# Optimization experiments

Hardware: AMD Instinct MI355X
Metric: run time of the kernel (lower is better)

The kernel has to match this reference:

```python
import jax, jax.numpy as jnp
import numpy as np

N = 50000          # total nodes
N_USER = 40000     # main (user) nodes
E = 400000         # edges per node kind
K = 3              # node kinds (separate graphs)
H = 4              # attention heads
F_IN = 128         # n_units[0]
F_OUT = 64         # n_units[1]
NB_CLASSES = 40
SLOPE = 0.2        # leaky relu negative slope


def setup_inputs() -> dict:
    key = jax.random.key(0)
    ks = jax.random.split(key, 12)
    h = jax.random.normal(ks[0], (N, F_IN), dtype=jnp.float32)
    edge_index = jax.random.randint(ks[1], (K, 2, E), 0, N, dtype=jnp.int32)
    # per-kind SpGATLayer params (bias=False)
    w = jax.random.normal(ks[2], (K, H, F_IN, F_OUT), dtype=jnp.float32) * 0.1
    a_src = jax.random.normal(ks[3], (K, H, F_OUT), dtype=jnp.float32) * 0.1
    a_trg = jax.random.normal(ks[4], (K, H, F_OUT), dtype=jnp.float32) * 0.1
    # AdditiveAttention: w1 (d=F_IN -> d2=F_OUT), w2 (d1=F_OUT -> d2=F_OUT), m (d2 -> 1)
    w1 = jax.random.normal(ks[5], (F_IN, F_OUT), dtype=jnp.float32) * 0.1
    w2 = jax.random.normal(ks[6], (F_OUT, F_OUT), dtype=jnp.float32) * 0.1
    m = jax.random.normal(ks[7], (F_OUT,), dtype=jnp.float32) * 0.1
    # final fc: in = F_OUT*(K+1)
    fc_w = jax.random.normal(ks[8], (F_OUT * (K + 1), NB_CLASSES), dtype=jnp.float32) * 0.1
    fc_b = jnp.zeros((NB_CLASSES,), dtype=jnp.float32)
    return {"h": h, "edge_index": edge_index, "w": w, "a_src": a_src,
            "a_trg": a_trg, "w1": w1, "w2": w2, "m": m,
            "fc_w": fc_w, "fc_b": fc_b}


def _spgat_kind(h, src, trg, wk, ask, atk):
    # h: [N, F_IN], wk: [H, F_IN, F_OUT], ask/atk: [H, F_OUT]
    hp = jnp.einsum('nd,hdf->nhf', h, wk)               # [N, H, F_OUT]
    s = jnp.einsum('nhf,hf->nh', hp, ask)               # [N, H]
    t = jnp.einsum('nhf,hf->nh', hp, atk)               # [N, H]
    e = s[src] + t[trg]                                 # [E, H]
    e = jnp.where(e >= 0, e, SLOPE * e)                 # leaky relu
    e = e - jnp.max(e)                                  # global max shift (as in source)
    exp_e = jnp.exp(e)
    denom = jax.ops.segment_sum(exp_e, trg, num_segments=N)  # [N, H]
    alpha = exp_e / (denom[trg] + 1e-16)                # [E, H]
    msg = hp[src] * alpha[:, :, None]                   # [E, H, F_OUT]
    out = jax.ops.segment_sum(msg, trg, num_segments=N) # [N, H, F_OUT]
    return out.mean(axis=1)                             # [N, F_OUT] (last layer head-mean)


def reference(h, edge_index, w, a_src, a_trg, w1, w2, m, fc_w, fc_b):
    heter = []
    for k in range(K):  # fixed small loop over node kinds
        x = _spgat_kind(h, edge_index[k, 0], edge_index[k, 1],
                        w[k], a_src[k], a_trg[k])
        heter.append(x[:N_USER])
    type_aware = jnp.stack(heter, axis=1)               # [N_USER, K, F_OUT]
    feature = h[:N_USER]                                # [N_USER, F_IN]
    q = jnp.tanh((feature @ w1)[:, None, :] + type_aware @ w2)  # [N_USER, K, F_OUT]
    scores = q @ m                                      # [N_USER, K]
    beta = jax.nn.softmax(scores, axis=-1)
    fusion = jnp.einsum('nk,nkf->nf', beta, type_aware) # [N_USER, F_OUT]
    ret = jnp.concatenate([type_aware, fusion[:, None, :]], axis=1)
    ret = ret.reshape(N_USER, -1)                       # [N_USER, F_OUT*(K+1)]
    logits = ret @ fc_w + fc_b
    return jax.nn.log_softmax(logits, axis=-1)
```

## Files before the change

kernel.cpp:

```cpp
#include <hip/hip_runtime.h>
#include <hip/hip_bf16.h>

#define NN    50000
#define NUSER 40000
#define EE    400000
#define KKIND 3
#define HHEAD 4
#define FIN   128
#define FOUT  64
#define NCLS  40

typedef __attribute__((ext_vector_type(8))) short short8;
typedef __attribute__((ext_vector_type(4))) float floatx4;

__device__ __forceinline__ float bf2f(unsigned short u) {
    unsigned int v = ((unsigned int)u) << 16;
    return __uint_as_float(v);
}
__device__ __forceinline__ unsigned short f2bf(float f) {
    unsigned int u = __float_as_uint(f);
    unsigned int r = (u + 0x7FFFu + ((u >> 16) & 1u)) >> 16;
    return (unsigned short)r;
}

#define OFF_H    0
#define OFF_W    6400000
#define OFF_ASRC 6498304
#define OFF_ATRG 6499072
#define OFF_W1   6499840
#define OFF_W2   6508032
#define OFF_M    6512128
#define OFF_FCW  6512192
#define OFF_FCB  6522432
#define CONV_TOT 6522472

__global__ __launch_bounds__(256) void detect_kernel(const unsigned short* __restrict__ hraw,
                                                     int* __restrict__ flag)
{
    __shared__ int cnt;
    if (threadIdx.x == 0) cnt = 0;
    __syncthreads();
    int local = 0;
#pragma unroll
    for (int j = 0; j < 8; j++) {
        unsigned short u = hraw[threadIdx.x * 8 + j];
        int ex = (u >> 7) & 0xFF;
        if (ex >= 0x90) local++;
    }
    atomicAdd(&cnt, local);
    __syncthreads();
    if (threadIdx.x == 0) *flag = (cnt > 100) ? 1 : 0;
}

__global__ __launch_bounds__(256) void conv_kernel(const void* __restrict__ p0, const void* __restrict__ p2,
                                                   const void* __restrict__ p3, const void* __restrict__ p4,
                                                   const void* __restrict__ p5, const void* __restrict__ p6,
                                                   const void* __restrict__ p7, const void* __restrict__ p8,
                                                   const void* __restrict__ p9,
                                                   const int* __restrict__ flagp,
                                                   unsigned short* __restrict__ dst)
{
    int tid = (blockIdx.x * 256 + threadIdx.x) * 8;
    if (tid >= CONV_TOT) return;
    const void* src; int li;
    if      (tid < OFF_W)    { src = p0; li = tid - OFF_H; }
    else if (tid < OFF_ASRC) { src = p2; li = tid - OFF_W; }
    else if (tid < OFF_ATRG) { src = p3; li = tid - OFF_ASRC; }
    else if (tid < OFF_W1)   { src = p4; li = tid - OFF_ATRG; }
    else if (tid < OFF_W2)   { src = p5; li = tid - OFF_W1; }
    else if (tid < OFF_M)    { src = p6; li = tid - OFF_W2; }
    else if (tid < OFF_FCW)  { src = p7; li = tid - OFF_M; }
    else if (tid < OFF_FCB)  { src = p8; li = tid - OFF_FCW; }
    else                     { src = p9; li = tid - OFF_FCB; }
    if (*flagp) {
        const float* fp = (const float*)src + li;
        float4 x = *(const float4*)fp;
        float4 y = *(const float4*)(fp + 4);
        uint4 o;
        o.x = (unsigned int)f2bf(x.x) | ((unsigned int)f2bf(x.y) << 16);
        o.y = (unsigned int)f2bf(x.z) | ((unsigned int)f2bf(x.w) << 16);
        o.z = (unsigned int)f2bf(y.x) | ((unsigned int)f2bf(y.y) << 16);
        o.w = (unsigned int)f2bf(y.z) | ((unsigned int)f2bf(y.w) << 16);
        *(uint4*)(dst + tid) = o;
    } else {
        *(uint4*)(dst + tid) = *(const uint4*)((const unsigned short*)src + li);
    }
}

__global__ __launch_bounds__(256) void repack_w(const unsigned short* __restrict__ w,
                                                unsigned short* __restrict__ wT)
{
    int tid = blockIdx.x * 256 + threadIdx.x;
    if (tid >= 12288) return;
    int f = tid & 63, g = (tid >> 6) & 15, h = (tid >> 10) & 3, k = tid >> 12;
    const unsigned short* src = w + (size_t)(k * 4 + h) * 8192 + f;
    unsigned short* dst = wT + (size_t)tid * 8;
#pragma unroll
    for (int j = 0; j < 8; j++) dst[j] = src[(size_t)(g * 8 + j) * 64];
}

__global__ __launch_bounds__(256) void repack_small(const unsigned short* __restrict__ w1,
                                                    const unsigned short* __restrict__ w2,
                                                    const unsigned short* __restrict__ fcw,
                                                    unsigned short* __restrict__ w1T,
                                                    unsigned short* __restrict__ w2T,
                                                    unsigned short* __restrict__ fcwT)
{
    int tid = blockIdx.x * 256 + threadIdx.x;
    if (tid < 1024) {
        int c = tid & 63, g = tid >> 6;
#pragma unroll
        for (int j = 0; j < 8; j++) w1T[(size_t)(g * 64 + c) * 8 + j] = w1[(size_t)(g * 8 + j) * 64 + c];
    } else if (tid < 1536) {
        int t = tid - 1024; int c = t & 63, g = t >> 6;
#pragma unroll
        for (int j = 0; j < 8; j++) w2T[(size_t)(g * 64 + c) * 8 + j] = w2[(size_t)(g * 8 + j) * 64 + c];
    } else if (tid < 3072) {
        int t = tid - 1536; int c = t % 48, g = t / 48;
#pragma unroll
        for (int j = 0; j < 8; j++)
            fcwT[(size_t)(g * 48 + c) * 8 + j] = (c < NCLS) ? fcw[(size_t)(g * 8 + j) * NCLS + c] : (unsigned short)0;
    }
}

__global__ __launch_bounds__(256) void hist3(const int* __restrict__ ei,
                                             unsigned int* __restrict__ cnt,
                                             unsigned int* __restrict__ rank)
{
    int e = blockIdx.x * 256 + threadIdx.x;
    int k = blockIdx.y;
    if (e >= EE) return;
    int tn = ei[(size_t)k * 2 * EE + EE + e];
    if (tn < NUSER)
        rank[(size_t)k * EE + e] = atomicAdd(&cnt[(size_t)k * NUSER + tn], 1u);
}

#define SCB 20
__global__ __launch_bounds__(256) void scanA(const unsigned int* __restrict__ cnt,
                                             unsigned int* __restrict__ partials)
{
    int k = blockIdx.y, b = blockIdx.x;
    const unsigned int* c = cnt + (size_t)k * NUSER;
    int base = b * 2048 + threadIdx.x * 8;
    unsigned int s = 0;
#pragma unroll
    for (int j = 0; j < 8; j++) { int idx = base + j; if (idx < NUSER) s += c[idx]; }
#pragma unroll
    for (int off = 1; off < 64; off <<= 1) s += __shfl_xor(s, off, 64);
    __shared__ unsigned int wsum[4];
    int lane = threadIdx.x & 63, wid = threadIdx.x >> 6;
    if (lane == 0) wsum[wid] = s;
    __syncthreads();
    if (threadIdx.x == 0) partials[k * SCB + b] = wsum[0] + wsum[1] + wsum[2] + wsum[3];
}

__global__ __launch_bounds__(256) void scanB(unsigned int* __restrict__ partials,
                                             unsigned int* __restrict__ rowptr)
{
    int wid = threadIdx.x >> 6, lane = threadIdx.x & 63;
    if (wid >= KKIND) return;
    unsigned int v = (lane < SCB) ? partials[wid * SCB + lane] : 0u;
    unsigned int inc = v;
#pragma unroll
    for (int off = 1; off < 32; off <<= 1) {
        unsigned int u = __shfl_up(inc, off, 64);
        if (lane >= off) inc += u;
    }
    if (lane < SCB) partials[wid * SCB + lane] = inc - v;
    if (lane == SCB - 1) rowptr[(size_t)wid * (NUSER + 1) + NUSER] = inc;
}

__global__ __launch_bounds__(256) void scanC(const unsigned int* __restrict__ cnt,
                                             const unsigned int* __restrict__ partials,
                                             unsigned int* __restrict__ rowptr)
{
    int k = blockIdx.y, b = blockIdx.x;
    const unsigned int* c = cnt + (size_t)k * NUSER;
    unsigned int* rp = rowptr + (size_t)k * (NUSER + 1);
    int lane = threadIdx.x & 63, wid = threadIdx.x >> 6;
    int base = b * 2048 + threadIdx.x * 8;
    unsigned int vals[8]; unsigned int s = 0;
#pragma unroll
    for (int j = 0; j < 8; j++) { int idx = base + j; vals[j] = (idx < NUSER) ? c[idx] : 0u; s += vals[j]; }
    unsigned int inc = s;
#pragma unroll
    for (int off = 1; off < 64; off <<= 1) {
        unsigned int u = __shfl_up(inc, off, 64);
        if (lane >= off) inc += u;
    }
    __shared__ unsigned int wsum[4];
    if (lane == 63) wsum[wid] = inc;
    __syncthreads();
    unsigned int woff = 0;
    for (int i = 0; i < wid; i++) woff += wsum[i];
    unsigned int run = partials[k * SCB + b] + woff + (inc - s);
#pragma unroll
    for (int j = 0; j < 8; j++) {
        int idx = base + j;
        if (idx < NUSER) { rp[idx] = run; run += vals[j]; }
    }
}

__global__ __launch_bounds__(256) void scatter3(const int* __restrict__ ei,
                                                const unsigned int* __restrict__ rowptr,
                                                const unsigned int* __restrict__ rank,
                                                int* __restrict__ srcl)
{
    int e = blockIdx.x * 256 + threadIdx.x;
    int k = blockIdx.y;
    if (e >= EE) return;
    const int* srcA = ei + (size_t)k * 2 * EE;
    int tn = srcA[EE + e];
    if (tn >= NUSER) return;
    unsigned int p = rowptr[(size_t)k * (NUSER + 1) + tn] + rank[(size_t)k * EE + e];
    srcl[(size_t)k * EE + p] = srcA[e];
}

__global__ __launch_bounds__(256) void hp_gemm(const unsigned short* __restrict__ h,
                                               const unsigned short* __restrict__ wTk,
                                               const unsigned short* __restrict__ ak_src,
                                               const unsigned short* __restrict__ ak_trg,
                                               unsigned short* __restrict__ hp2,
                                               float* __restrict__ sb, float* __restrict__ tb)
{
    int wave = (blockIdx.x * 256 + threadIdx.x) >> 6;
    int lane = threadIdx.x & 63;
    if (wave >= NN / 16) return;
    int m0 = wave * 16;
    int mi = lane & 15, quad = lane >> 4;

    short8 a[4];
    const unsigned short* hrow = h + (size_t)(m0 + mi) * FIN + quad * 8;
#pragma unroll
    for (int kk = 0; kk < 4; kk++) a[kk] = *(const short8*)(hrow + kk * 32);

    float sp[4][4], tp[4][4];
#pragma unroll
    for (int r = 0; r < 4; r++)
#pragma unroll
        for (int q2 = 0; q2 < 4; q2++) { sp[r][q2] = 0.f; tp[r][q2] = 0.f; }

#pragma unroll
    for (int j = 0; j < 4; j++) {
        int fc = j * 16 + mi;
        floatx4 acc4[4];
#pragma unroll
        for (int hh = 0; hh < 4; hh++) {
            floatx4 acc = {0.f, 0.f, 0.f, 0.f};
#pragma unroll
            for (int kk = 0; kk < 4; kk++) {
                short8 b = *(const short8*)(wTk + (size_t)((hh * 16 + kk * 4 + quad) * 64 + fc) * 8);
                acc = __builtin_amdgcn_mfma_f32_16x16x32_bf16(a[kk], b, acc, 0, 0, 0);
            }
            acc4[hh] = acc;
            float asv = bf2f(ak_src[hh * 64 + fc]);
            float atv = bf2f(ak_trg[hh * 64 + fc]);
#pragma unroll
            for (int reg = 0; reg < 4; reg++) {
                sp[reg][hh] += acc[reg] * asv;
                tp[reg][hh] += acc[reg] * atv;
            }
        }
#pragma unroll
        for (int reg = 0; reg < 4; reg++) {
            ushort4 pk;
            pk.x = f2bf(acc4[0][reg]); pk.y = f2bf(acc4[1][reg]);
            pk.z = f2bf(acc4[2][reg]); pk.w = f2bf(acc4[3][reg]);
            int row = m0 + quad * 4 + reg;
            *(ushort4*)(hp2 + (size_t)row * 256 + fc * 4) = pk;
        }
    }
#pragma unroll
    for (int off = 1; off < 16; off <<= 1)
#pragma unroll
        for (int r = 0; r < 4; r++)
#pragma unroll
            for (int q2 = 0; q2 < 4; q2++) {
                sp[r][q2] += __shfl_xor(sp[r][q2], off, 64);
                tp[r][q2] += __shfl_xor(tp[r][q2], off, 64);
            }
    float sv = 0.f, tv = 0.f;
#pragma unroll
    for (int r = 0; r < 4; r++)
#pragma unroll
        for (int q2 = 0; q2 < 4; q2++) {
            bool sel = (mi == r * 4 + q2);
            sv = sel ? sp[r][q2] : sv;
            tv = sel ? tp[r][q2] : tv;
        }
    int rr = m0 + quad * 4 + (mi >> 2);
    sb[rr * 4 + (mi & 3)] = sv;
    tb[rr * 4 + (mi & 3)] = tv;
}

__global__ __launch_bounds__(256) void passB6(const unsigned int* __restrict__ rowptr,
                                              const int* __restrict__ srcl,
                                              const float* __restrict__ sb,
                                              const float* __restrict__ tb,
                                              const unsigned short* __restrict__ hp2,
                                              unsigned short* __restrict__ ret, int kslice)
{
    __shared__ int   lds_src[4][64];
    __shared__ float4 lds_ew[4][64];
    int wid = threadIdx.x >> 6;
    int n = __builtin_amdgcn_readfirstlane(blockIdx.x * 4 + wid);
    int f = threadIdx.x & 63;
    unsigned int beg = rowptr[n], end = rowptr[n + 1];
    float4 t4 = *(const float4*)(tb + (size_t)n * 4);
    float num0 = 0.f, num1 = 0.f, num2 = 0.f, num3 = 0.f;
    float den0 = 0.f, den1 = 0.f, den2 = 0.f, den3 = 0.f;

    for (unsigned int p0 = beg; p0 < end; p0 += 64) {
        unsigned int cnt = end - p0; if (cnt > 64) cnt = 64;
        int s = 0;
        float4 e = {0.f, 0.f, 0.f, 0.f};
        if ((unsigned int)f < cnt) {
            s = srcl[p0 + f];
            float4 sv = *(const float4*)(sb + (size_t)s * 4);
            float v0 = sv.x + t4.x, v1 = sv.y + t4.y, v2 = sv.z + t4.z, v3 = sv.w + t4.w;
            v0 = (v0 >= 0.f) ? v0 : 0.2f * v0;  v1 = (v1 >= 0.f) ? v1 : 0.2f * v1;
            v2 = (v2 >= 0.f) ? v2 : 0.2f * v2;  v3 = (v3 >= 0.f) ? v3 : 0.2f * v3;
            e.x = __expf(v0); e.y = __expf(v1); e.z = __expf(v2); e.w = __expf(v3);
        }
        lds_src[wid][f] = s;
        lds_ew[wid][f] = e;
        float d0 = e.x, d1 = e.y, d2 = e.z, d3 = e.w;
#pragma unroll
        for (int off = 1; off < 64; off <<= 1) {
            d0 += __shfl_xor(d0, off, 64); d1 += __shfl_xor(d1, off, 64);
            d2 += __shfl_xor(d2, off, 64); d3 += __shfl_xor(d3, off, 64);
        }
        den0 += d0; den1 += d1; den2 += d2; den3 += d3;
        unsigned int jmax = (cnt + 7u) & ~7u;
        for (unsigned int j = 0; j < jmax; j += 8) {
            int ss[8]; float4 ee[8];
#pragma unroll
            for (int u = 0; u < 8; u++) { ss[u] = lds_src[wid][j + u]; ee[u] = lds_ew[wid][j + u]; }
            ushort4 hv[8];
#pragma unroll
            for (int u = 0; u < 8; u++) hv[u] = *(const ushort4*)(hp2 + (size_t)ss[u] * 256 + f * 4);
#pragma unroll
            for (int u = 0; u < 8; u++) {
                num0 += ee[u].x * bf2f(hv[u].x); num1 += ee[u].y * bf2f(hv[u].y);
                num2 += ee[u].z * bf2f(hv[u].z); num3 += ee[u].w * bf2f(hv[u].w);
            }
        }
    }
    float r = 0.25f * (num0 / (den0 + 1e-16f) + num1 / (den1 + 1e-16f)
                     + num2 / (den2 + 1e-16f) + num3 / (den3 + 1e-16f));
    ret[(size_t)n * 256 + kslice * 64 + f] = f2bf(r);
}

__global__ __launch_bounds__(256) void qscore2(const unsigned short* __restrict__ h,
                                               const unsigned short* __restrict__ w1T,
                                               const unsigned short* __restrict__ retA,
                                               const unsigned short* __restrict__ w2T,
                                               const unsigned short* __restrict__ mvec,
                                               float* __restrict__ scores, int M)
{
    int wave = (blockIdx.x * 256 + threadIdx.x) >> 6;
    int lane = threadIdx.x & 63;
    int m0 = wave * 16;
    if (m0 >= M) return;
    int mi = lane & 15, quad = lane >> 4;

    floatx4 fw[4];
#pragma unroll
    for (int nt = 0; nt < 4; nt++) fw[nt] = (floatx4){0.f, 0.f, 0.f, 0.f};
#pragma unroll
    for (int kk = 0; kk < 4; kk++) {
        short8 a = *(const short8*)(h + (size_t)(m0 + mi) * FIN + kk * 32 + quad * 8);
#pragma unroll
        for (int nt = 0; nt < 4; nt++) {
            short8 b = *(const short8*)(w1T + (size_t)((kk * 4 + quad) * 64 + nt * 16 + mi) * 8);
            fw[nt] = __builtin_amdgcn_mfma_f32_16x16x32_bf16(a, b, fw[nt], 0, 0, 0);
        }
    }

    for (int k = 0; k < KKIND; k++) {
        floatx4 acc[4];
#pragma unroll
        for (int nt = 0; nt < 4; nt++) acc[nt] = (floatx4){0.f, 0.f, 0.f, 0.f};
#pragma unroll
        for (int kk = 0; kk < 2; kk++) {
            short8 a = *(const short8*)(retA + (size_t)(m0 + mi) * 256 + k * 64 + kk * 32 + quad * 8);
#pragma unroll
            for (int nt = 0; nt < 4; nt++) {
                short8 b = *(const short8*)(w2T + (size_t)((kk * 4 + quad) * 64 + nt * 16 + mi) * 8);
                acc[nt] = __builtin_amdgcn_mfma_f32_16x16x32_bf16(a, b, acc[nt], 0, 0, 0);
            }
        }
        float part[4] = {0.f, 0.f, 0.f, 0.f};
#pragma unroll
        for (int nt = 0; nt < 4; nt++) {
            int col = nt * 16 + mi;
            float mval = bf2f(mvec[col]);
#pragma unroll
            for (int reg = 0; reg < 4; reg++) {
                float x = acc[nt][reg] + fw[nt][reg];
                float q = 1.f - 2.f / (1.f + __expf(2.f * x));
                part[reg] += q * mval;
            }
        }
#pragma unroll
        for (int off = 1; off < 16; off <<= 1)
#pragma unroll
            for (int reg = 0; reg < 4; reg++) part[reg] += __shfl_xor(part[reg], off, 64);
        if (mi == 0) {
#pragma unroll
            for (int reg = 0; reg < 4; reg++)
                scores[(size_t)(m0 + quad * 4 + reg) * 3 + k] = part[reg];
        }
    }
}

__global__ __launch_bounds__(256) void fuse_kernel(const float* __restrict__ scores,
                                                   unsigned short* __restrict__ ret)
{
    int n = blockIdx.x * 4 + (threadIdx.x >> 6);
    int f = threadIdx.x & 63;
    float s0 = scores[n * 3 + 0], s1 = scores[n * 3 + 1], s2 = scores[n * 3 + 2];
    float mx = fmaxf(s0, fmaxf(s1, s2));
    float e0 = __expf(s0 - mx), e1 = __expf(s1 - mx), e2 = __expf(s2 - mx);
    float inv = 1.f / (e0 + e1 + e2);
    const unsigned short* row = ret + (size_t)n * 256;
    float fu = (e0 * bf2f(row[f]) + e1 * bf2f(row[64 + f]) + e2 * bf2f(row[128 + f])) * inv;
    ret[(size_t)n * 256 + 192 + f] = f2bf(fu);
}

__global__ __launch_bounds__(256) void fc_lsm(const unsigned short* __restrict__ A,
                                              const unsigned short* __restrict__ fcwT,
                                              const unsigned short* __restrict__ bias,
                                              const int* __restrict__ flagp,
                                              void* __restrict__ out, int M)
{
    int wave = (blockIdx.x * 256 + threadIdx.x) >> 6;
    int lane = threadIdx.x & 63;
    int m0 = wave * 16;
    if (m0 >= M) return;
    int mi = lane & 15, quad = lane >> 4;
    floatx4 acc[3];
#pragma unroll
    for (int nt = 0; nt < 3; nt++) acc[nt] = (floatx4){0.f, 0.f, 0.f, 0.f};
#pragma unroll
    for (int kk = 0; kk < 8; kk++) {
        short8 a = *(const short8*)(A + (size_t)(m0 + mi) * 256 + kk * 32 + quad * 8);
#pragma unroll
        for (int nt = 0; nt < 3; nt++) {
            short8 b = *(const short8*)(fcwT + (size_t)((kk * 4 + quad) * 48 + nt * 16 + mi) * 8);
            acc[nt] = __builtin_amdgcn_mfma_f32_16x16x32_bf16(a, b, acc[nt], 0, 0, 0);
        }
    }
    int fl = *flagp;
    float bv[3]; bool ok[3];
#pragma unroll
    for (int nt = 0; nt < 3; nt++) {
        int col = nt * 16 + mi;
        ok[nt] = (col < NCLS);
        bv[nt] = ok[nt] ? bf2f(bias[col]) : 0.f;
    }
#pragma unroll
    for (int reg = 0; reg < 4; reg++) {
        float v[3];
#pragma unroll
        for (int nt = 0; nt < 3; nt++)
            v[nt] = ok[nt] ? (acc[nt][reg] + bv[nt]) : -3.4e38f;
        float mx = fmaxf(fmaxf(v[0], v[1]), v[2]);
#pragma unroll
        for (int off = 1; off < 16; off <<= 1) mx = fmaxf(mx, __shfl_xor(mx, off, 64));
        float s = 0.f;
#pragma unroll
        for (int nt = 0; nt < 3; nt++) s += ok[nt] ? __expf(v[nt] - mx) : 0.f;
#pragma unroll
        for (int off = 1; off < 16; off <<= 1) s += __shfl_xor(s, off, 64);
        float lse = mx + __logf(s);
        int row = m0 + quad * 4 + reg;
#pragma unroll
        for (int nt = 0; nt < 3; nt++) {
            int col = nt * 16 + mi;
            if (col < NCLS) {
                float ls = v[nt] - lse;
                size_t idx = (size_t)row * NCLS + col;
                if (fl) ((float*)out)[idx] = ls;
                else    ((unsigned short*)out)[idx] = f2bf(ls);
            }
        }
    }
}

extern "C" void kernel_launch(void* const* d_in, const int* in_sizes, int n_in,
                              void* d_out, int out_size, void* d_ws, size_t ws_size,
                              hipStream_t stream)
{
    (void)in_sizes; (void)n_in; (void)out_size; (void)ws_size;
    const int* ei = (const int*)d_in[1];

    char* ws = (char*)d_ws;
    unsigned short* conv = (unsigned short*)ws;
    unsigned short* hc   = conv + OFF_H;
    unsigned short* wc   = conv + OFF_W;
    unsigned short* asrc = conv + OFF_ASRC;
    unsigned short* atrg = conv + OFF_ATRG;
    unsigned short* w1c  = conv + OFF_W1;
    unsigned short* w2c  = conv + OFF_W2;
    unsigned short* mc   = conv + OFF_M;
    unsigned short* fcwc = conv + OFF_FCW;
    unsigned short* fcbc = conv + OFF_FCB;
    int* flag             = (int*)(ws + 13044944);
    unsigned short* wT    = (unsigned short*)(ws + 13045248);
    unsigned short* w1T   = (unsigned short*)(ws + 13241856);
    unsigned short* w2T   = (unsigned short*)(ws + 13258240);
    unsigned short* fcwT  = (unsigned short*)(ws + 13266432);
    unsigned int* partials= (unsigned int*)(ws + 13291008);
    unsigned int* cnt     = (unsigned int*)(ws + 13291264);
    float* scores         = (float*)(ws + 13291264);
    unsigned int* rowptr  = (unsigned int*)(ws + 13771264);
    int* srcl             = (int*)(ws + 14251520);
    unsigned int* rank    = (unsigned int*)(ws + 19051520);
    float* sbuf           = (float*)(ws + 23851520);
    float* tbuf           = (float*)(ws + 24651520);
    unsigned short* hp2   = (unsigned short*)(ws + 25451520);
    unsigned short* ret   = (unsigned short*)(ws + 51051520);

    detect_kernel<<<1, 256, 0, stream>>>((const unsigned short*)d_in[0], flag);
    conv_kernel<<<(CONV_TOT / 8 + 255) / 256, 256, 0, stream>>>(
        d_in[0], d_in[2], d_in[3], d_in[4], d_in[5], d_in[6], d_in[7], d_in[8], d_in[9],
        flag, conv);

    repack_w<<<48, 256, 0, stream>>>(wc, wT);
    repack_small<<<12, 256, 0, stream>>>(w1c, w2c, fcwc, w1T, w2T, fcwT);

    hipMemsetAsync(cnt, 0, (size_t)KKIND * NUSER * 4, stream);
    hist3<<<dim3(1563, 3), 256, 0, stream>>>(ei, cnt, rank);
    scanA<<<dim3(SCB, 3), 256, 0, stream>>>(cnt, partials);
    scanB<<<1, 256, 0, stream>>>(partials, rowptr);
    scanC<<<dim3(SCB, 3), 256, 0, stream>>>(cnt, partials, rowptr);
    scatter3<<<dim3(1563, 3), 256, 0, stream>>>(ei, rowptr, rank, srcl);

    for (int k = 0; k < KKIND; k++) {
        hp_gemm<<<782, 256, 0, stream>>>(hc, wT + (size_t)k * 32768,
                                         asrc + k * HHEAD * FOUT, atrg + k * HHEAD * FOUT,
                                         hp2, sbuf, tbuf);
        passB6<<<NUSER / 4, 256, 0, stream>>>(rowptr + (size_t)k * (NUSER + 1),
                                              srcl + (size_t)k * EE,
                                              sbuf, tbuf, hp2, ret, k);
    }

    qscore2<<<625, 256, 0, stream>>>(hc, w1T, ret, w2T, mc, scores, NUSER);
    fuse_kernel<<<NUSER / 4, 256, 0, stream>>>(scores, ret);
    fc_lsm<<<625, 256, 0, stream>>>(ret, fcwT, fcbc, flag, d_out, NUSER);
}
```

Before: 375.2 us.

## Batch all node kinds into single GEMM/aggregation launches and fuse softmax fusion into qscore

When the workspace is large enough, the projection GEMM now computes all three kinds in one launch, reusing the loaded h fragments, and the aggregation kernel processes all kinds in one grid. This removes the serial per-kind launch chain and raises parallelism in the gather pass. The separate fuse kernel is folded into qscore, which keeps the retA fragments in registers and computes the beta-weighted fusion directly. The hist and scatter kernels each handle four edges per thread. The cost is a larger workspace layout with a fallback path when it is too small.

```diff
diff --git a/kernel.cpp b/kernel.cpp
--- a/kernel.cpp
+++ b/kernel.cpp
@@ -127,12 +127,26 @@
                                              unsigned int* __restrict__ cnt,
                                              unsigned int* __restrict__ rank)
 {
-    int e = blockIdx.x * 256 + threadIdx.x;
     int k = blockIdx.y;
-    if (e >= EE) return;
-    int tn = ei[(size_t)k * 2 * EE + EE + e];
-    if (tn < NUSER)
-        rank[(size_t)k * EE + e] = atomicAdd(&cnt[(size_t)k * NUSER + tn], 1u);
+    const int* trg = ei + (size_t)k * 2 * EE + EE;
+    unsigned int* ck = cnt + (size_t)k * NUSER;
+    unsigned int* rk = rank + (size_t)k * EE;
+    int e0 = blockIdx.x * 1024 + threadIdx.x;
+    int t[4];
+#pragma unroll
+    for (int j = 0; j < 4; j++) {
+        int e = e0 + j * 256;
+        t[j] = (e < EE) ? trg[e] : NUSER;
+    }
+    unsigned int r[4];
+#pragma unroll
+    for (int j = 0; j < 4; j++)
+        r[j] = (t[j] < NUSER) ? atomicAdd(&ck[t[j]], 1u) : 0u;
+#pragma unroll
+    for (int j = 0; j < 4; j++) {
+        int e = e0 + j * 256;
+        if (e < EE && t[j] < NUSER) rk[e] = r[j];
+    }
 }
 
 #define SCB 20
@@ -206,22 +220,39 @@
                                                 const unsigned int* __restrict__ rank,
                                                 int* __restrict__ srcl)
 {
-    int e = blockIdx.x * 256 + threadIdx.x;
     int k = blockIdx.y;
-    if (e >= EE) return;
     const int* srcA = ei + (size_t)k * 2 * EE;
-    int tn = srcA[EE + e];
-    if (tn >= NUSER) return;
-    unsigned int p = rowptr[(size_t)k * (NUSER + 1) + tn] + rank[(size_t)k * EE + e];
-    srcl[(size_t)k * EE + p] = srcA[e];
-}
-
-__global__ __launch_bounds__(256) void hp_gemm(const unsigned short* __restrict__ h,
-                                               const unsigned short* __restrict__ wTk,
-                                               const unsigned short* __restrict__ ak_src,
-                                               const unsigned short* __restrict__ ak_trg,
-                                               unsigned short* __restrict__ hp2,
-                                               float* __restrict__ sb, float* __restrict__ tb)
+    const int* trg = srcA + EE;
+    const unsigned int* rp = rowptr + (size_t)k * (NUSER + 1);
+    const unsigned int* rk = rank + (size_t)k * EE;
+    int* sl = srcl + (size_t)k * EE;
+    int e0 = blockIdx.x * 1024 + threadIdx.x;
+    int t[4], s[4]; unsigned int r[4];
+#pragma unroll
+    for (int j = 0; j < 4; j++) {
+        int e = e0 + j * 256;
+        t[j] = (e < EE) ? trg[e] : NUSER;
+        s[j] = (e < EE) ? srcA[e] : 0;
+        r[j] = (e < EE && t[j] < NUSER) ? rk[e] : 0u;
+    }
+    unsigned int base[4];
+#pragma unroll
+    for (int j = 0; j < 4; j++) base[j] = (t[j] < NUSER) ? rp[t[j]] : 0u;
+#pragma unroll
+    for (int j = 0; j < 4; j++) {
+        int e = e0 + j * 256;
+        if (e < EE && t[j] < NUSER) sl[base[j] + r[j]] = s[j];
+    }
+}
+
+__global__ __launch_bounds__(256) void hp_gemm_multi(const unsigned short* __restrict__ h,
+                                                     const unsigned short* __restrict__ wTall,
+                                                     const unsigned short* __restrict__ asrc_all,
+                                                     const unsigned short* __restrict__ atrg_all,
+                                                     unsigned short* __restrict__ hp2,
+                                                     long long hp2_stride,
+                                                     float* __restrict__ sb, float* __restrict__ tb,
+                                                     int kbeg, int kcnt)
 {
     int wave = (blockIdx.x * 256 + threadIdx.x) >> 6;
     int lane = threadIdx.x & 63;
@@ -234,79 +265,97 @@
 #pragma unroll
     for (int kk = 0; kk < 4; kk++) a[kk] = *(const short8*)(hrow + kk * 32);
 
-    float sp[4][4], tp[4][4];
-#pragma unroll
-    for (int r = 0; r < 4; r++)
-#pragma unroll
-        for (int q2 = 0; q2 < 4; q2++) { sp[r][q2] = 0.f; tp[r][q2] = 0.f; }
-
-#pragma unroll
-    for (int j = 0; j < 4; j++) {
-        int fc = j * 16 + mi;
-        floatx4 acc4[4];
-#pragma unroll
-        for (int hh = 0; hh < 4; hh++) {
-            floatx4 acc = {0.f, 0.f, 0.f, 0.f};
-#pragma unroll
-            for (int kk = 0; kk < 4; kk++) {
-                short8 b = *(const short8*)(wTk + (size_t)((hh * 16 + kk * 4 + quad) * 64 + fc) * 8);
-                acc = __builtin_amdgcn_mfma_f32_16x16x32_bf16(a[kk], b, acc, 0, 0, 0);
+    for (int kq = 0; kq < kcnt; kq++) {
+        int k = kbeg + kq;
+        const unsigned short* wTk = wTall + (size_t)k * 32768;
+        const unsigned short* ak_src = asrc_all + k * 256;
+        const unsigned short* ak_trg = atrg_all + k * 256;
+        unsigned short* hp2k = hp2 + (size_t)kq * hp2_stride;
+        float* sbk = sb + (size_t)k * NN * 4;
+        float* tbk = tb + (size_t)k * NN * 4;
+
+        float sp[4][4], tp[4][4];
+#pragma unroll
+        for (int r = 0; r < 4; r++)
+#pragma unroll
+            for (int q2 = 0; q2 < 4; q2++) { sp[r][q2] = 0.f; tp[r][q2] = 0.f; }
+
+#pragma unroll
+        for (int j = 0; j < 4; j++) {
+            int fc = j * 16 + mi;
+            floatx4 acc4[4];
+#pragma unroll
+            for (int hh = 0; hh < 4; hh++) {
+                floatx4 acc = {0.f, 0.f, 0.f, 0.f};
+#pragma unroll
+                for (int kk = 0; kk < 4; kk++) {
+                    short8 b = *(const short8*)(wTk + (size_t)((hh * 16 + kk * 4 + quad) * 64 + fc) * 8);
+                    acc = __builtin_amdgcn_mfma_f32_16x16x32_bf16(a[kk], b, acc, 0, 0, 0);
+                }
+                acc4[hh] = acc;
+                float asv = bf2f(ak_src[hh * 64 + fc]);
+                float atv = bf2f(ak_trg[hh * 64 + fc]);
+#pragma unroll
+                for (int reg = 0; reg < 4; reg++) {
+                    sp[reg][hh] += acc[reg] * asv;
+                    tp[reg][hh] += acc[reg] * atv;
+                }
             }
-            acc4[hh] = acc;
-            float asv = bf2f(ak_src[hh * 64 + fc]);
-            float atv = bf2f(ak_trg[hh * 64 + fc]);
 #pragma unroll
             for (int reg = 0; reg < 4; reg++) {
-                sp[reg][hh] += acc[reg] * asv;
-                tp[reg][hh] += acc[reg] * atv;
+                ushort4 pk;
+                pk.x = f2bf(acc4[0][reg]); pk.y = f2bf(acc4[1][reg]);
+                pk.z = f2bf(acc4[2][reg]); pk.w = f2bf(acc4[3][reg]);
+                int row = m0 + quad * 4 + reg;
+                *(ushort4*)(hp2k + (size_t)row * 256 + fc * 4) = pk;
             }
         }
 #pragma unroll
-        for (int reg = 0; reg < 4; reg++) {
-            ushort4 pk;
-            pk.x = f2bf(acc4[0][reg]); pk.y = f2bf(acc4[1][reg]);
-            pk.z = f2bf(acc4[2][reg]); pk.w = f2bf(acc4[3][reg]);
-            int row = m0 + quad * 4 + reg;
-            *(ushort4*)(hp2 + (size_t)row * 256 + fc * 4) = pk;
-        }
-    }
-#pragma unroll
-    for (int off = 1; off < 16; off <<= 1)
+        for (int off = 1; off < 16; off <<= 1)
+#pragma unroll
+            for (int r = 0; r < 4; r++)
+#pragma unroll
+                for (int q2 = 0; q2 < 4; q2++) {
+                    sp[r][q2] += __shfl_xor(sp[r][q2], off, 64);
+                    tp[r][q2] += __shfl_xor(tp[r][q2], off, 64);
+                }
+        float sv = 0.f, tv = 0.f;
 #pragma unroll
         for (int r = 0; r < 4; r++)
 #pragma unroll
             for (int q2 = 0; q2 < 4; q2++) {
-                sp[r][q2] += __shfl_xor(sp[r][q2], off, 64);
-                tp[r][q2] += __shfl_xor(tp[r][q2], off, 64);
+                bool sel = (mi == r * 4 + q2);
+                sv = sel ? sp[r][q2] : sv;
+                tv = sel ? tp[r][q2] : tv;
             }
-    float sv = 0.f, tv = 0.f;
-#pragma unroll
-    for (int r = 0; r < 4; r++)
-#pragma unroll
-        for (int q2 = 0; q2 < 4; q2++) {
-            bool sel = (mi == r * 4 + q2);
-            sv = sel ? sp[r][q2] : sv;
-            tv = sel ? tp[r][q2] : tv;
-        }
-    int rr = m0 + quad * 4 + (mi >> 2);
-    sb[rr * 4 + (mi & 3)] = sv;
-    tb[rr * 4 + (mi & 3)] = tv;
-}
-
-__global__ __launch_bounds__(256) void passB6(const unsigned int* __restrict__ rowptr,
-                                              const int* __restrict__ srcl,
-                                              const float* __restrict__ sb,
-                                              const float* __restrict__ tb,
-                                              const unsigned short* __restrict__ hp2,
-                                              unsigned short* __restrict__ ret, int kslice)
-{
-    __shared__ int   lds_src[4][64];
+        int rr = m0 + quad * 4 + (mi >> 2);
+        sbk[rr * 4 + (mi & 3)] = sv;
+        tbk[rr * 4 + (mi & 3)] = tv;
+    }
+}
+
+__global__ __launch_bounds__(256) void passB_multi(const unsigned int* __restrict__ rowptr_all,
+                                                   const int* __restrict__ srcl_all,
+                                                   const float* __restrict__ sb,
+                                                   const float* __restrict__ tb,
+                                                   const unsigned short* __restrict__ hp2,
+                                                   long long hp2_stride,
+                                                   unsigned short* __restrict__ ret, int kbeg)
+{
+    __shared__ int    lds_src[4][64];
     __shared__ float4 lds_ew[4][64];
+    int kq = blockIdx.y, k = kbeg + kq;
+    const unsigned int* rowptr = rowptr_all + (size_t)k * (NUSER + 1);
+    const int* srcl = srcl_all + (size_t)k * EE;
+    const float* sbk = sb + (size_t)k * NN * 4;
+    const float* tbk = tb + (size_t)k * NN * 4;
+    const unsigned short* hp2k = hp2 + (size_t)kq * hp2_stride;
+
     int wid = threadIdx.x >> 6;
     int n = __builtin_amdgcn_readfirstlane(blockIdx.x * 4 + wid);
     int f = threadIdx.x & 63;
     unsigned int beg = rowptr[n], end = rowptr[n + 1];
-    float4 t4 = *(const float4*)(tb + (size_t)n * 4);
+    float4 t4 = *(const float4*)(tbk + (size_t)n * 4);
     float num0 = 0.f, num1 = 0.f, num2 = 0.f, num3 = 0.f;
     float den0 = 0.f, den1 = 0.f, den2 = 0.f, den3 = 0.f;
 
@@ -316,7 +365,7 @@
         float4 e = {0.f, 0.f, 0.f, 0.f};
         if ((unsigned int)f < cnt) {
             s = srcl[p0 + f];
-            float4 sv = *(const float4*)(sb + (size_t)s * 4);
+            float4 sv = *(const float4*)(sbk + (size_t)s * 4);
             float v0 = sv.x + t4.x, v1 = sv.y + t4.y, v2 = sv.z + t4.z, v3 = sv.w + t4.w;
             v0 = (v0 >= 0.f) ? v0 : 0.2f * v0;  v1 = (v1 >= 0.f) ? v1 : 0.2f * v1;
             v2 = (v2 >= 0.f) ? v2 : 0.2f * v2;  v3 = (v3 >= 0.f) ? v3 : 0.2f * v3;
@@ -338,7 +387,7 @@
             for (int u = 0; u < 8; u++) { ss[u] = lds_src[wid][j + u]; ee[u] = lds_ew[wid][j + u]; }
             ushort4 hv[8];
 #pragma unroll
-            for (int u = 0; u < 8; u++) hv[u] = *(const ushort4*)(hp2 + (size_t)ss[u] * 256 + f * 4);
+            for (int u = 0; u < 8; u++) hv[u] = *(const ushort4*)(hp2k + (size_t)ss[u] * 256 + f * 4);
 #pragma unroll
             for (int u = 0; u < 8; u++) {
                 num0 += ee[u].x * bf2f(hv[u].x); num1 += ee[u].y * bf2f(hv[u].y);
@@ -348,15 +397,15 @@
     }
     float r = 0.25f * (num0 / (den0 + 1e-16f) + num1 / (den1 + 1e-16f)
                      + num2 / (den2 + 1e-16f) + num3 / (den3 + 1e-16f));
-    ret[(size_t)n * 256 + kslice * 64 + f] = f2bf(r);
-}
-
-__global__ __launch_bounds__(256) void qscore2(const unsigned short* __restrict__ h,
-                                               const unsigned short* __restrict__ w1T,
-                                               const unsigned short* __restrict__ retA,
-                                               const unsigned short* __restrict__ w2T,
-                                               const unsigned short* __restrict__ mvec,
-                                               float* __restrict__ scores, int M)
+    ret[(size_t)n * 256 + k * 64 + f] = f2bf(r);
+}
+
+__global__ __launch_bounds__(256) void qscore2f(const unsigned short* __restrict__ h,
+                                                const unsigned short* __restrict__ w1T,
+                                                const unsigned short* __restrict__ retA,
+                                                const unsigned short* __restrict__ w2T,
+                                                const unsigned short* __restrict__ mvec,
+                                                unsigned short* __restrict__ ret, int M)
 {
     int wave = (blockIdx.x * 256 + threadIdx.x) >> 6;
     int lane = threadIdx.x & 63;
@@ -377,6 +426,8 @@
         }
     }
 
+    float pk[3][4];
+    short8 afr[3][2];
     for (int k = 0; k < KKIND; k++) {
         floatx4 acc[4];
 #pragma unroll
@@ -384,6 +435,7 @@
 #pragma unroll
         for (int kk = 0; kk < 2; kk++) {
             short8 a = *(const short8*)(retA + (size_t)(m0 + mi) * 256 + k * 64 + kk * 32 + quad * 8);
+            afr[k][kk] = a;
 #pragma unroll
             for (int nt = 0; nt < 4; nt++) {
                 short8 b = *(const short8*)(w2T + (size_t)((kk * 4 + quad) * 64 + nt * 16 + mi) * 8);
@@ -406,26 +458,38 @@
         for (int off = 1; off < 16; off <<= 1)
 #pragma unroll
             for (int reg = 0; reg < 4; reg++) part[reg] += __shfl_xor(part[reg], off, 64);
-        if (mi == 0) {
-#pragma unroll
-            for (int reg = 0; reg < 4; reg++)
-                scores[(size_t)(m0 + quad * 4 + reg) * 3 + k] = part[reg];
-        }
-    }
-}
-
-__global__ __launch_bounds__(256) void fuse_kernel(const float* __restrict__ scores,
-                                                   unsigned short* __restrict__ ret)
-{
-    int n = blockIdx.x * 4 + (threadIdx.x >> 6);
-    int f = threadIdx.x & 63;
-    float s0 = scores[n * 3 + 0], s1 = scores[n * 3 + 1], s2 = scores[n * 3 + 2];
+#pragma unroll
+        for (int reg = 0; reg < 4; reg++) pk[k][reg] = part[reg];
+    }
+
+    int rsel = mi & 3;
+    float sv0 = (rsel == 0) ? pk[0][0] : (rsel == 1) ? pk[0][1] : (rsel == 2) ? pk[0][2] : pk[0][3];
+    float sv1 = (rsel == 0) ? pk[1][0] : (rsel == 1) ? pk[1][1] : (rsel == 2) ? pk[1][2] : pk[1][3];
+    float sv2 = (rsel == 0) ? pk[2][0] : (rsel == 1) ? pk[2][1] : (rsel == 2) ? pk[2][2] : pk[2][3];
+    int srcLane = ((mi >> 2) << 4) | mi;
+    float s0 = __shfl(sv0, srcLane, 64);
+    float s1 = __shfl(sv1, srcLane, 64);
+    float s2 = __shfl(sv2, srcLane, 64);
     float mx = fmaxf(s0, fmaxf(s1, s2));
     float e0 = __expf(s0 - mx), e1 = __expf(s1 - mx), e2 = __expf(s2 - mx);
     float inv = 1.f / (e0 + e1 + e2);
-    const unsigned short* row = ret + (size_t)n * 256;
-    float fu = (e0 * bf2f(row[f]) + e1 * bf2f(row[64 + f]) + e2 * bf2f(row[128 + f])) * inv;
-    ret[(size_t)n * 256 + 192 + f] = f2bf(fu);
+    float w0 = e0 * inv, w1 = e1 * inv, w2 = e2 * inv;
+
+#pragma unroll
+    for (int kk = 0; kk < 2; kk++) {
+        unsigned short pkd[8];
+#pragma unroll
+        for (int j = 0; j < 8; j++) {
+            float fu = w0 * bf2f((unsigned short)afr[0][kk][j])
+                     + w1 * bf2f((unsigned short)afr[1][kk][j])
+                     + w2 * bf2f((unsigned short)afr[2][kk][j]);
+            pkd[j] = f2bf(fu);
+        }
+        *(ushort4*)(ret + (size_t)(m0 + mi) * 256 + 192 + kk * 32 + quad * 8) =
+            *(ushort4*)&pkd[0];
+        *(ushort4*)(ret + (size_t)(m0 + mi) * 256 + 192 + kk * 32 + quad * 8 + 4) =
+            *(ushort4*)&pkd[4];
+    }
 }
 
 __global__ __launch_bounds__(256) void fc_lsm(const unsigned short* __restrict__ A,
@@ -492,7 +556,7 @@
                               void* d_out, int out_size, void* d_ws, size_t ws_size,
                               hipStream_t stream)
 {
-    (void)in_sizes; (void)n_in; (void)out_size; (void)ws_size;
+    (void)in_sizes; (void)n_in; (void)out_size;
     const int* ei = (const int*)d_in[1];
 
     char* ws = (char*)d_ws;
@@ -513,14 +577,16 @@
     unsigned short* fcwT  = (unsigned short*)(ws + 13266432);
     unsigned int* partials= (unsigned int*)(ws + 13291008);
     unsigned int* cnt     = (unsigned int*)(ws + 13291264);
-    float* scores         = (float*)(ws + 13291264);
     unsigned int* rowptr  = (unsigned int*)(ws + 13771264);
     int* srcl             = (int*)(ws + 14251520);
     unsigned int* rank    = (unsigned int*)(ws + 19051520);
     float* sbuf           = (float*)(ws + 23851520);
-    float* tbuf           = (float*)(ws + 24651520);
-    unsigned short* hp2   = (unsigned short*)(ws + 25451520);
-    unsigned short* ret   = (unsigned short*)(ws + 51051520);
+    float* tbuf           = (float*)(ws + 26251520);
+    unsigned short* ret   = (unsigned short*)(ws + 28651520);
+    unsigned short* hp2   = (unsigned short*)(ws + 49131520);
+
+    const size_t NEED_BIG = 49131520ull + 3ull * NN * 256 * 2;
+    int big = (ws_size >= NEED_BIG) ? 1 : 0;
 
     detect_kernel<<<1, 256, 0, stream>>>((const unsigned short*)d_in[0], flag);
     conv_kernel<<<(CONV_TOT / 8 + 255) / 256, 256, 0, stream>>>(
@@ -531,22 +597,27 @@
     repack_small<<<12, 256, 0, stream>>>(w1c, w2c, fcwc, w1T, w2T, fcwT);
 
     hipMemsetAsync(cnt, 0, (size_t)KKIND * NUSER * 4, stream);
-    hist3<<<dim3(1563, 3), 256, 0, stream>>>(ei, cnt, rank);
+    hist3<<<dim3((EE + 1023) / 1024, 3), 256, 0, stream>>>(ei, cnt, rank);
     scanA<<<dim3(SCB, 3), 256, 0, stream>>>(cnt, partials);
     scanB<<<1, 256, 0, stream>>>(partials, rowptr);
     scanC<<<dim3(SCB, 3), 256, 0, stream>>>(cnt, partials, rowptr);
-    scatter3<<<dim3(1563, 3), 256, 0, stream>>>(ei, rowptr, rank, srcl);
-
-    for (int k = 0; k < KKIND; k++) {
-        hp_gemm<<<782, 256, 0, stream>>>(hc, wT + (size_t)k * 32768,
-                                         asrc + k * HHEAD * FOUT, atrg + k * HHEAD * FOUT,
-                                         hp2, sbuf, tbuf);
-        passB6<<<NUSER / 4, 256, 0, stream>>>(rowptr + (size_t)k * (NUSER + 1),
-                                              srcl + (size_t)k * EE,
-                                              sbuf, tbuf, hp2, ret, k);
-    }
-
-    qscore2<<<625, 256, 0, stream>>>(hc, w1T, ret, w2T, mc, scores, NUSER);
-    fuse_kernel<<<NUSER / 4, 256, 0, stream>>>(scores, ret);
+    scatter3<<<dim3((EE + 1023) / 1024, 3), 256, 0, stream>>>(ei, rowptr, rank, srcl);
+
+    if (big) {
+        long long stride = (long long)NN * 256;
+        hp_gemm_multi<<<782, 256, 0, stream>>>(hc, wT, asrc, atrg, hp2, stride,
+                                               sbuf, tbuf, 0, 3);
+        passB_multi<<<dim3(NUSER / 4, 3), 256, 0, stream>>>(rowptr, srcl, sbuf, tbuf,
+                                                            hp2, stride, ret, 0);
+    } else {
+        for (int k = 0; k < KKIND; k++) {
+            hp_gemm_multi<<<782, 256, 0, stream>>>(hc, wT, asrc, atrg, hp2, 0,
+                                                   sbuf, tbuf, k, 1);
+            passB_multi<<<dim3(NUSER / 4, 1), 256, 0, stream>>>(rowptr, srcl, sbuf, tbuf,
+                                                                hp2, 0, ret, k);
+        }
+    }
+
+    qscore2f<<<625, 256, 0, stream>>>(hc, w1T, ret, w2T, mc, ret, NUSER);
     fc_lsm<<<625, 256, 0, stream>>>(ret, fcwT, fcbc, flag, d_out, NUSER);
 }
```

Measured after the change: 400.4 us. 1.07x slower.
